# Performance work log

Hardware: AMD Instinct MI355X
Metric: run time of the kernel (lower is better)

## Reference

```python
import jax, jax.numpy as jnp
import numpy as np

N_IM, N_OBJ = 16, 16          # images, objects per image
D_IN = 2048                    # obj_pair_feat_dim
PER_IM = N_OBJ * (N_OBJ + 1) // 2   # obj boxes + union boxes per image
N_BOX = N_IM * PER_IM               # 2176
N_PAIR = N_IM * N_OBJ * (N_OBJ - 1) # is_ex=True -> 2*C(n,2) per image = 3840
NUM_REL = 3


def setup_inputs() -> dict:
    rng = np.random.default_rng(0)
    H, W = 600.0, 800.0
    boxes = np.zeros((N_BOX, 5), np.float32)
    o1i, o2i, ui, imi = [], [], [], []
    for i in range(N_IM):
        off = i * PER_IM
        x1 = rng.uniform(0, W / 2, N_OBJ); y1 = rng.uniform(0, H / 2, N_OBJ)
        bw = rng.uniform(10, W / 2, N_OBJ); bh = rng.uniform(10, H / 2, N_OBJ)
        boxes[off:off + N_OBJ] = np.stack([np.full(N_OBJ, i), x1, y1, x1 + bw, y1 + bh], 1)
        uc = off + N_OBJ
        for a in range(N_OBJ):
            for b in range(a + 1, N_OBJ):
                boxes[uc] = [i, min(x1[a], x1[b]), min(y1[a], y1[b]),
                             max(x1[a] + bw[a], x1[b] + bw[b]), max(y1[a] + bh[a], y1[b] + bh[b])]
                o1i += [off + a, off + b]; o2i += [off + b, off + a]
                ui += [uc, uc]; imi += [i, i]
                uc += 1
    im_info = np.tile(np.array([H, W, 1.0], np.float32), (N_IM, 1))
    key = jax.random.key(0)
    ks = jax.random.split(key, 16)
    lin = lambda k, i, o: jax.random.normal(k, (i, o), jnp.float32) * 0.02
    return dict(
        xs=jax.random.normal(ks[0], (N_PAIR, D_IN), jnp.float32) * 0.1,
        xo=jax.random.normal(ks[1], (N_PAIR, D_IN), jnp.float32) * 0.1,
        xu=jax.random.normal(ks[2], (N_PAIR, D_IN), jnp.float32) * 0.1,
        boxes=jnp.asarray(boxes), im_info=jnp.asarray(im_info),
        o1_idx=jnp.asarray(o1i, jnp.int32), o2_idx=jnp.asarray(o2i, jnp.int32),
        u_idx=jnp.asarray(ui, jnp.int32), img_idx=jnp.asarray(imi, jnp.int32),
        Ws1=lin(ks[3], D_IN, 512), bs1=jnp.zeros(512, jnp.float32),
        Ws2=lin(ks[4], 512, 256), bs2=jnp.zeros(256, jnp.float32),
        Wo1=lin(ks[5], D_IN, 512), bo1=jnp.zeros(512, jnp.float32),
        Wo2=lin(ks[6], 512, 256), bo2=jnp.zeros(256, jnp.float32),
        Wu1=lin(ks[7], D_IN, 512), bu1=jnp.zeros(512, jnp.float32),
        Wu2=lin(ks[8], 512, 256), bu2=jnp.zeros(256, jnp.float32),
        Wc1=lin(ks[9], 256 + 19, 256), bc1=jnp.zeros(256, jnp.float32),
        Wc2=lin(ks[10], 256, NUM_REL), bc2=jnp.zeros(NUM_REL, jnp.float32),
    )


def _mlp(x, W1, b1, W2, b2):
    return jax.nn.relu(jax.nn.relu(x @ W1 + b1) @ W2 + b2)


def _encode_loc(sb, ob, ub, hw):
    # sb/ob/ub: [P,4] (x1,y1,x2,y2); hw: [P,2] (h_i, w_i)
    h_i, w_i = hw[:, 0], hw[:, 1]
    x_s = (sb[:, 0] + sb[:, 2]) / 2.0; y_s = (sb[:, 1] + sb[:, 3]) / 2.0
    w_s = sb[:, 2] - sb[:, 0]; h_s = sb[:, 3] - sb[:, 1]
    x_o = (ob[:, 0] + ob[:, 2]) / 2.0; y_o = (ob[:, 1] + ob[:, 3]) / 2.0
    w_o = ob[:, 2] - ob[:, 0]; h_o = ob[:, 3] - ob[:, 1]
    a_s = w_s * h_s; a_o = w_o * h_o
    a_u = (ub[:, 2] - ub[:, 0]) * (ub[:, 3] - ub[:, 1])
    area = w_i * h_i
    return jnp.stack([
        x_s / w_i, y_s / h_i, (x_s + w_s) / w_i, (y_s + h_s) / h_i, a_s / area,
        x_o / w_i, y_o / h_i, (x_o + w_o) / w_i, (y_o + h_o) / h_i, a_o / area,
        (x_s - x_o) / w_o, (y_s - y_o) / h_o, jnp.log(w_s / w_o), jnp.log(h_s / h_o),
        (x_o - x_s) / w_s, (y_o - y_s) / h_s, jnp.log(w_o / w_s), jnp.log(h_o / h_s),
        a_u / area], axis=1)  # [P,19]


def reference(xs, xo, xu, boxes, im_info, o1_idx, o2_idx, u_idx, img_idx,
              Ws1, bs1, Ws2, bs2, Wo1, bo1, Wo2, bo2, Wu1, bu1, Wu2, bu2,
              Wc1, bc1, Wc2, bc2):
    fs = _mlp(xs, Ws1, bs1, Ws2, bs2)
    fo = _mlp(xo, Wo1, bo1, Wo2, bo2)
    fu = _mlp(xu, Wu1, bu1, Wu2, bu2)
    appear = fu - fo - fs                              # [P,256]
    loc = _encode_loc(boxes[o1_idx, 1:5], boxes[o2_idx, 1:5],
                      boxes[u_idx, 1:5], im_info[img_idx, :2])  # [P,19]
    h = jax.nn.relu(jnp.concatenate([appear, loc], axis=1) @ Wc1 + bc1)
    return h @ Wc2 + bc2                               # [P,num_rel]
```

## Files before the change

### kernel.cpp

```cpp
#include <hip/hip_runtime.h>

#define N_PAIR 3840

typedef short bf16x8 __attribute__((ext_vector_type(8)));
typedef float f32x4 __attribute__((ext_vector_type(4)));

static __device__ __forceinline__ ushort f2bf(float f) {
    uint x = __float_as_uint(f);
    uint r = (x + 0x7FFFu + ((x >> 16) & 1u)) >> 16;
    return (ushort)r;
}
static __device__ __forceinline__ float bf2f(ushort u) {
    return __uint_as_float(((uint)u) << 16);
}

__global__ void transpose_convert(const float* __restrict__ in0,
                                  const float* __restrict__ in1,
                                  const float* __restrict__ in2,
                                  ushort* __restrict__ out,
                                  int K, int N, int Kpad) {
    const float* in = (blockIdx.z == 0) ? in0 : (blockIdx.z == 1 ? in1 : in2);
    ushort* o = out + (size_t)blockIdx.z * N * Kpad;
    __shared__ float tile[64][65];
    int k0 = blockIdx.x * 64, n0 = blockIdx.y * 64;
    int t = threadIdx.x;
    int r = t >> 2, c4 = (t & 3) * 16;
#pragma unroll
    for (int i = 0; i < 16; i++) {
        int k = k0 + r, n = n0 + c4 + i;
        tile[r][c4 + i] = (k < K && n < N) ? in[(size_t)k * N + n] : 0.f;
    }
    __syncthreads();
#pragma unroll
    for (int i = 0; i < 16; i++) {
        int n = n0 + r, k = k0 + c4 + i;
        if (n < N && k < Kpad) o[(size_t)n * Kpad + k] = f2bf(tile[c4 + i][r]);
    }
}

__global__ void transpose_convert2(const float* __restrict__ Ws2,
                                   const float* __restrict__ Wo2,
                                   const float* __restrict__ Wu2,
                                   const float* __restrict__ Wc1,
                                   ushort* __restrict__ W2T,
                                   ushort* __restrict__ WC1T) {
    int z = blockIdx.z;
    const float* in; ushort* o; int K, N, Kpad;
    if (z < 3) {
        in = (z == 0) ? Ws2 : (z == 1 ? Wo2 : Wu2);
        o = W2T + (size_t)z * 256 * 512; K = 512; N = 256; Kpad = 512;
    } else {
        in = Wc1; o = WC1T; K = 275; N = 256; Kpad = 288;
    }
    __shared__ float tile[64][65];
    int k0 = blockIdx.x * 64, n0 = blockIdx.y * 64;
    int t = threadIdx.x;
    int r = t >> 2, c4 = (t & 3) * 16;
#pragma unroll
    for (int i = 0; i < 16; i++) {
        int k = k0 + r, n = n0 + c4 + i;
        tile[r][c4 + i] = (k < K && n < N) ? in[(size_t)k * N + n] : 0.f;
    }
    __syncthreads();
#pragma unroll
    for (int i = 0; i < 16; i++) {
        int n = n0 + r, k = k0 + c4 + i;
        if (n < N && k < Kpad) o[(size_t)n * Kpad + k] = f2bf(tile[c4 + i][r]);
    }
}

__device__ __forceinline__ bf16x8 frag_ld(const ushort* __restrict__ lds, int row, int colbyte) {
    int off = (row << 7) + (colbyte ^ ((row & 7) << 4));
    return *reinterpret_cast<const bf16x8*>(reinterpret_cast<const char*>(lds) + off);
}
__device__ __forceinline__ bf16x8 frag32_ld(const ushort* __restrict__ lds, int row, int colbyte) {
    int off = (row << 6) + (colbyte ^ ((row & 3) << 4));
    return *reinterpret_cast<const bf16x8*>(reinterpret_cast<const char*>(lds) + off);
}

__global__ __launch_bounds__(256) void gemm1(const float* __restrict__ xs,
                                             const float* __restrict__ xo,
                                             const float* __restrict__ xu,
                                             const ushort* __restrict__ w1t,
                                             const float* __restrict__ b_s,
                                             const float* __restrict__ b_o,
                                             const float* __restrict__ b_u,
                                             ushort* __restrict__ h1out) {
    int br = blockIdx.z;
    const float* x = br == 0 ? xs : (br == 1 ? xo : xu);
    const ushort* wt = w1t + (size_t)br * 512 * 2048;
    const float* bias = br == 0 ? b_s : (br == 1 ? b_o : b_u);
    ushort* out = h1out + (size_t)br * 3840 * 512;

    __shared__ ushort As[2][64 * 64];
    __shared__ ushort Bs[2][128 * 64];
    int t = threadIdx.x, lane = t & 63, wid = t >> 6;
    int wr = wid >> 1, wc = wid & 1;
    int m0 = blockIdx.x * 64, n0 = blockIdx.y * 128;
    const float* asrc = x + (size_t)m0 * 2048;
    const ushort* bsrc = wt + (size_t)n0 * 2048;

    int ar = t >> 2, ac = (t & 3) * 16;
    float4 pa[4];
    bf16x8 pb[4];

    auto issue = [&](int kt) {
        const float4* g = reinterpret_cast<const float4*>(asrc + (size_t)ar * 2048 + kt + ac);
#pragma unroll
        for (int i = 0; i < 4; i++) pa[i] = g[i];
#pragma unroll
        for (int it = 0; it < 4; it++) {
            int e = (it * 256 + t) * 8;
            int rr = e >> 6, cc = e & 63;
            pb[it] = *reinterpret_cast<const bf16x8*>(bsrc + (size_t)rr * 2048 + kt + cc);
        }
    };
    auto commit = [&](int buf) {
        union { bf16x8 v; ushort us[8]; } p0, p1;
#pragma unroll
        for (int i = 0; i < 4; i++) {
            p0.us[i] = f2bf(pa[0][i]); p0.us[4 + i] = f2bf(pa[1][i]);
            p1.us[i] = f2bf(pa[2][i]); p1.us[4 + i] = f2bf(pa[3][i]);
        }
        char* ab = reinterpret_cast<char*>(&As[buf][0]);
        int off0 = (ar << 7) + (((ac) << 1) ^ ((ar & 7) << 4));
        int off1 = (ar << 7) + (((ac + 8) << 1) ^ ((ar & 7) << 4));
        *reinterpret_cast<bf16x8*>(ab + off0) = p0.v;
        *reinterpret_cast<bf16x8*>(ab + off1) = p1.v;
        char* bb = reinterpret_cast<char*>(&Bs[buf][0]);
#pragma unroll
        for (int it = 0; it < 4; it++) {
            int e = (it * 256 + t) * 8;
            int rr = e >> 6, cc = e & 63;
            int off = (rr << 7) + ((cc << 1) ^ ((rr & 7) << 4));
            *reinterpret_cast<bf16x8*>(bb + off) = pb[it];
        }
    };

    f32x4 acc[2][4] = {};
    issue(0);
    commit(0);
    __syncthreads();
    int cur = 0;
    for (int kt = 0; kt < 2048; kt += 64) {
        int nxt = kt + 64;
        if (nxt < 2048) issue(nxt);
#pragma unroll
        for (int kk = 0; kk < 64; kk += 32) {
            int cb = (kk + ((lane >> 4) << 3)) << 1;
            bf16x8 a[2], b[4];
#pragma unroll
            for (int i = 0; i < 2; i++) a[i] = frag_ld(&As[cur][0], wr * 32 + i * 16 + (lane & 15), cb);
#pragma unroll
            for (int f = 0; f < 4; f++) b[f] = frag_ld(&Bs[cur][0], wc * 64 + f * 16 + (lane & 15), cb);
#pragma unroll
            for (int i = 0; i < 2; i++)
#pragma unroll
                for (int j = 0; j < 4; j++)
                    acc[i][j] = __builtin_amdgcn_mfma_f32_16x16x32_bf16(a[i], b[j], acc[i][j], 0, 0, 0);
        }
        if (nxt < 2048) commit(cur ^ 1);
        __syncthreads();
        cur ^= 1;
    }
    int rb = m0 + wr * 32 + ((lane >> 4) << 2);
    int cb0 = n0 + wc * 64 + (lane & 15);
#pragma unroll
    for (int j = 0; j < 4; j++) {
        int col = cb0 + j * 16;
        float bv = bias[col];
#pragma unroll
        for (int i = 0; i < 2; i++)
#pragma unroll
            for (int q = 0; q < 4; q++) {
                int row = rb + i * 16 + q;
                float v = acc[i][j][q] + bv;
                v = v > 0.f ? v : 0.f;
                out[(size_t)row * 512 + col] = f2bf(v);
            }
    }
}

__global__ __launch_bounds__(256) void gemm2(const ushort* __restrict__ h1,
                                             const ushort* __restrict__ w2t,
                                             const float* __restrict__ b_s,
                                             const float* __restrict__ b_o,
                                             const float* __restrict__ b_u,
                                             ushort* __restrict__ h2br) {
    int br = blockIdx.z;
    const ushort* A = h1 + (size_t)br * 3840 * 512;
    const ushort* B = w2t + (size_t)br * 256 * 512;
    const float* bias = br == 0 ? b_s : (br == 1 ? b_o : b_u);
    ushort* out = h2br + (size_t)br * 3840 * 256;

    __shared__ ushort As[2][64 * 64];
    __shared__ ushort Bs[2][128 * 64];
    int t = threadIdx.x, lane = t & 63, wid = t >> 6;
    int wr = wid >> 1, wc = wid & 1;
    int m0 = blockIdx.x * 64, n0 = blockIdx.y * 128;
    const ushort* asrc = A + (size_t)m0 * 512;
    const ushort* bsrc = B + (size_t)n0 * 512;

    int ar = t >> 2, ac = (t & 3) * 16;
    bf16x8 pa[2], pb[4];
    auto issue = [&](int kt) {
        const bf16x8* g = reinterpret_cast<const bf16x8*>(asrc + (size_t)ar * 512 + kt + ac);
        pa[0] = g[0]; pa[1] = g[1];
#pragma unroll
        for (int it = 0; it < 4; it++) {
            int e = (it * 256 + t) * 8;
            int rr = e >> 6, cc = e & 63;
            pb[it] = *reinterpret_cast<const bf16x8*>(bsrc + (size_t)rr * 512 + kt + cc);
        }
    };
    auto commit = [&](int buf) {
        char* ab = reinterpret_cast<char*>(&As[buf][0]);
        int off0 = (ar << 7) + ((ac << 1) ^ ((ar & 7) << 4));
        int off1 = (ar << 7) + (((ac + 8) << 1) ^ ((ar & 7) << 4));
        *reinterpret_cast<bf16x8*>(ab + off0) = pa[0];
        *reinterpret_cast<bf16x8*>(ab + off1) = pa[1];
        char* bb = reinterpret_cast<char*>(&Bs[buf][0]);
#pragma unroll
        for (int it = 0; it < 4; it++) {
            int e = (it * 256 + t) * 8;
            int rr = e >> 6, cc = e & 63;
            int off = (rr << 7) + ((cc << 1) ^ ((rr & 7) << 4));
            *reinterpret_cast<bf16x8*>(bb + off) = pb[it];
        }
    };

    f32x4 acc[2][4] = {};
    issue(0);
    commit(0);
    __syncthreads();
    int cur = 0;
    for (int kt = 0; kt < 512; kt += 64) {
        int nxt = kt + 64;
        if (nxt < 512) issue(nxt);
#pragma unroll
        for (int kk = 0; kk < 64; kk += 32) {
            int cb = (kk + ((lane >> 4) << 3)) << 1;
            bf16x8 a[2], b[4];
#pragma unroll
            for (int i = 0; i < 2; i++) a[i] = frag_ld(&As[cur][0], wr * 32 + i * 16 + (lane & 15), cb);
#pragma unroll
            for (int f = 0; f < 4; f++) b[f] = frag_ld(&Bs[cur][0], wc * 64 + f * 16 + (lane & 15), cb);
#pragma unroll
            for (int i = 0; i < 2; i++)
#pragma unroll
                for (int j = 0; j < 4; j++)
                    acc[i][j] = __builtin_amdgcn_mfma_f32_16x16x32_bf16(a[i], b[j], acc[i][j], 0, 0, 0);
        }
        if (nxt < 512) commit(cur ^ 1);
        __syncthreads();
        cur ^= 1;
    }
    int rb = m0 + wr * 32 + ((lane >> 4) << 2);
    int cb0 = n0 + wc * 64 + (lane & 15);
#pragma unroll
    for (int j = 0; j < 4; j++) {
        int col = cb0 + j * 16;
        float bv = bias[col];
#pragma unroll
        for (int i = 0; i < 2; i++)
#pragma unroll
            for (int q = 0; q < 4; q++) {
                int row = rb + i * 16 + q;
                float v = acc[i][j][q] + bv;
                v = v > 0.f ? v : 0.f;
                out[(size_t)row * 256 + col] = f2bf(v);
            }
    }
}

__global__ void appear_pack(const ushort* __restrict__ h2br,
                            ushort* __restrict__ hin,
                            const float* __restrict__ boxes,
                            const float* __restrict__ im_info,
                            const int* __restrict__ o1, const int* __restrict__ o2,
                            const int* __restrict__ u, const int* __restrict__ im) {
    int i = blockIdx.x * 256 + threadIdx.x;
    if (i < N_PAIR * 32) {
        int p = i >> 5, ch = (i & 31) * 8;
        const ushort* ps = h2br + (size_t)p * 256 + ch;
        bf16x8 vs = *reinterpret_cast<const bf16x8*>(ps);
        bf16x8 vo = *reinterpret_cast<const bf16x8*>(ps + (size_t)3840 * 256);
        bf16x8 vu = *reinterpret_cast<const bf16x8*>(ps + (size_t)2 * 3840 * 256);
        union { bf16x8 v; ushort us[8]; } r;
#pragma unroll
        for (int j = 0; j < 8; j++)
            r.us[j] = f2bf(bf2f(((ushort)vu[j])) - bf2f(((ushort)vo[j])) - bf2f(((ushort)vs[j])));
        *reinterpret_cast<bf16x8*>(hin + (size_t)p * 288 + ch) = r.v;
    }
    if (blockIdx.x < 15) {
        int p = blockIdx.x * 256 + threadIdx.x;
        const float* sb = boxes + 5 * o1[p] + 1;
        const float* ob = boxes + 5 * o2[p] + 1;
        const float* ub = boxes + 5 * u[p] + 1;
        const float* ii = im_info + 3 * im[p];
        float hi = ii[0], wi = ii[1];
        float x_s = (sb[0] + sb[2]) * 0.5f, y_s = (sb[1] + sb[3]) * 0.5f;
        float w_s = sb[2] - sb[0], h_s = sb[3] - sb[1];
        float x_o = (ob[0] + ob[2]) * 0.5f, y_o = (ob[1] + ob[3]) * 0.5f;
        float w_o = ob[2] - ob[0], h_o = ob[3] - ob[1];
        float a_s = w_s * h_s, a_o = w_o * h_o;
        float a_u = (ub[2] - ub[0]) * (ub[3] - ub[1]);
        float area = wi * hi;
        float f[19];
        f[0] = x_s / wi;            f[1] = y_s / hi;
        f[2] = (x_s + w_s) / wi;    f[3] = (y_s + h_s) / hi;
        f[4] = a_s / area;
        f[5] = x_o / wi;            f[6] = y_o / hi;
        f[7] = (x_o + w_o) / wi;    f[8] = (y_o + h_o) / hi;
        f[9] = a_o / area;
        f[10] = (x_s - x_o) / w_o;  f[11] = (y_s - y_o) / h_o;
        f[12] = logf(w_s / w_o);    f[13] = logf(h_s / h_o);
        f[14] = (x_o - x_s) / w_s;  f[15] = (y_o - y_s) / h_s;
        f[16] = logf(w_o / w_s);    f[17] = logf(h_o / h_s);
        f[18] = a_u / area;
        ushort* row = hin + (size_t)p * 288 + 256;
#pragma unroll
        for (int k = 0; k < 19; k++) row[k] = f2bf(f[k]);
#pragma unroll
        for (int k = 19; k < 32; k++) row[k] = 0;
    }
}

__global__ __launch_bounds__(256) void gemm3(const ushort* __restrict__ hin,
                                             const ushort* __restrict__ wc1t,
                                             const float* __restrict__ bc1,
                                             ushort* __restrict__ h2) {
    __shared__ ushort As[2][64 * 32];
    __shared__ ushort Bs[2][128 * 32];
    int t = threadIdx.x, lane = t & 63, wid = t >> 6;
    int wr = wid >> 1, wc = wid & 1;
    int m0 = blockIdx.x * 64, n0 = blockIdx.y * 128;
    const ushort* asrc = hin + (size_t)m0 * 288;
    const ushort* bsrc = wc1t + (size_t)n0 * 288;

    int ar = t >> 2, ac = (t & 3) * 8;
    bf16x8 pa, pb[2];
    auto issue = [&](int kt) {
        pa = *reinterpret_cast<const bf16x8*>(asrc + (size_t)ar * 288 + kt + ac);
#pragma unroll
        for (int it = 0; it < 2; it++) {
            int e = (it * 256 + t) * 8;
            int rr = e >> 5, cc = e & 31;
            pb[it] = *reinterpret_cast<const bf16x8*>(bsrc + (size_t)rr * 288 + kt + cc);
        }
    };
    auto commit = [&](int buf) {
        char* ab = reinterpret_cast<char*>(&As[buf][0]);
        int off0 = (ar << 6) + ((ac << 1) ^ ((ar & 3) << 4));
        *reinterpret_cast<bf16x8*>(ab + off0) = pa;
        char* bb = reinterpret_cast<char*>(&Bs[buf][0]);
#pragma unroll
        for (int it = 0; it < 2; it++) {
            int e = (it * 256 + t) * 8;
            int rr = e >> 5, cc = e & 31;
            int off = (rr << 6) + ((cc << 1) ^ ((rr & 3) << 4));
            *reinterpret_cast<bf16x8*>(bb + off) = pb[it];
        }
    };

    f32x4 acc[2][4] = {};
    issue(0);
    commit(0);
    __syncthreads();
    int cur = 0;
    for (int kt = 0; kt < 288; kt += 32) {
        int nxt = kt + 32;
        if (nxt < 288) issue(nxt);
        int cb = ((lane >> 4) << 3) << 1;
        bf16x8 a[2], b[4];
#pragma unroll
        for (int i = 0; i < 2; i++) a[i] = frag32_ld(&As[cur][0], wr * 32 + i * 16 + (lane & 15), cb);
#pragma unroll
        for (int f = 0; f < 4; f++) b[f] = frag32_ld(&Bs[cur][0], wc * 64 + f * 16 + (lane & 15), cb);
#pragma unroll
        for (int i = 0; i < 2; i++)
#pragma unroll
            for (int j = 0; j < 4; j++)
                acc[i][j] = __builtin_amdgcn_mfma_f32_16x16x32_bf16(a[i], b[j], acc[i][j], 0, 0, 0);
        if (nxt < 288) commit(cur ^ 1);
        __syncthreads();
        cur ^= 1;
    }
    int rb = m0 + wr * 32 + ((lane >> 4) << 2);
    int cb0 = n0 + wc * 64 + (lane & 15);
#pragma unroll
    for (int j = 0; j < 4; j++) {
        int col = cb0 + j * 16;
        float bv = bc1[col];
#pragma unroll
        for (int i = 0; i < 2; i++)
#pragma unroll
            for (int q = 0; q < 4; q++) {
                int row = rb + i * 16 + q;
                float v = acc[i][j][q] + bv;
                v = v > 0.f ? v : 0.f;
                h2[(size_t)row * 256 + col] = f2bf(v);
            }
    }
}

__global__ void final_fc(const ushort* __restrict__ h2,
                         const float* __restrict__ wc2,
                         const float* __restrict__ bc2,
                         float* __restrict__ out) {
    __shared__ float w[768];
    int t = threadIdx.x;
    for (int i = t; i < 768; i += 256) w[i] = wc2[i];
    __syncthreads();
    int g = t >> 4, l = t & 15;
    int row = blockIdx.x * 16 + g;
    const ushort* hr = h2 + (size_t)row * 256 + l * 16;
    bf16x8 v0 = *reinterpret_cast<const bf16x8*>(hr);
    bf16x8 v1 = *reinterpret_cast<const bf16x8*>(hr + 8);
    float s0 = 0.f, s1 = 0.f, s2 = 0.f;
#pragma unroll
    for (int k = 0; k < 8; k++) {
        float h = bf2f((ushort)v0[k]);
        int c = (l * 16 + k) * 3;
        s0 += h * w[c]; s1 += h * w[c + 1]; s2 += h * w[c + 2];
    }
#pragma unroll
    for (int k = 0; k < 8; k++) {
        float h = bf2f((ushort)v1[k]);
        int c = (l * 16 + 8 + k) * 3;
        s0 += h * w[c]; s1 += h * w[c + 1]; s2 += h * w[c + 2];
    }
#pragma unroll
    for (int m = 1; m < 16; m <<= 1) {
        s0 += __shfl_xor(s0, m);
        s1 += __shfl_xor(s1, m);
        s2 += __shfl_xor(s2, m);
    }
    if (l == 0) {
        out[row * 3 + 0] = s0 + bc2[0];
        out[row * 3 + 1] = s1 + bc2[1];
        out[row * 3 + 2] = s2 + bc2[2];
    }
}

extern "C" void kernel_launch(void* const* d_in, const int* in_sizes, int n_in,
                              void* d_out, int out_size, void* d_ws, size_t ws_size,
                              hipStream_t stream) {
    (void)in_sizes; (void)n_in; (void)out_size; (void)ws_size;
    const float* xs = (const float*)d_in[0];
    const float* xo = (const float*)d_in[1];
    const float* xu = (const float*)d_in[2];
    const float* boxes = (const float*)d_in[3];
    const float* im_info = (const float*)d_in[4];
    const int* o1 = (const int*)d_in[5];
    const int* o2 = (const int*)d_in[6];
    const int* uu = (const int*)d_in[7];
    const int* im = (const int*)d_in[8];
    const float* Ws1 = (const float*)d_in[9];
    const float* bs1 = (const float*)d_in[10];
    const float* Ws2 = (const float*)d_in[11];
    const float* bs2 = (const float*)d_in[12];
    const float* Wo1 = (const float*)d_in[13];
    const float* bo1 = (const float*)d_in[14];
    const float* Wo2 = (const float*)d_in[15];
    const float* bo2 = (const float*)d_in[16];
    const float* Wu1 = (const float*)d_in[17];
    const float* bu1 = (const float*)d_in[18];
    const float* Wu2 = (const float*)d_in[19];
    const float* bu2 = (const float*)d_in[20];
    const float* Wc1 = (const float*)d_in[21];
    const float* bc1 = (const float*)d_in[22];
    const float* Wc2 = (const float*)d_in[23];
    const float* bc2 = (const float*)d_in[24];
    float* out = (float*)d_out;

    ushort* W1T = (ushort*)d_ws;
    ushort* H2BR = W1T;
    ushort* W2T = W1T + (size_t)3 * 512 * 2048;
    ushort* WC1T = W2T + (size_t)3 * 256 * 512;
    ushort* H1 = WC1T + (size_t)256 * 288;
    ushort* HIN = H1 + (size_t)3 * 3840 * 512;
    ushort* H2 = HIN + (size_t)3840 * 288;

    transpose_convert<<<dim3(32, 8, 3), 256, 0, stream>>>(Ws1, Wo1, Wu1, W1T, 2048, 512, 2048);
    transpose_convert2<<<dim3(8, 4, 4), 256, 0, stream>>>(Ws2, Wo2, Wu2, Wc1, W2T, WC1T);
    gemm1<<<dim3(60, 4, 3), 256, 0, stream>>>(xs, xo, xu, W1T, bs1, bo1, bu1, H1);
    gemm2<<<dim3(60, 2, 3), 256, 0, stream>>>(H1, W2T, bs2, bo2, bu2, H2BR);
    appear_pack<<<480, 256, 0, stream>>>(H2BR, HIN, boxes, im_info, o1, o2, uu, im);
    gemm3<<<dim3(60, 2), 256, 0, stream>>>(HIN, WC1T, bc1, H2);
    final_fc<<<240, 256, 0, stream>>>(H2, Wc2, bc2, out);
}
```

Baseline: 105.0 us.

## Remap GEMM blocks XCD-aware and prefetch two K-tiles ahead in registers

Both MLP GEMMs now use a flat 1D grid with a remap so that consecutive blocks on the same XCD (bid&7) cover contiguous tiles of the same branch, aiming for better L2 reuse of A rows and weight tiles. The main loop is also unrolled by two with two register staging sets, so global loads for tile k+2 are issued while tile k is computed, deepening the prefetch distance. This raises register pressure and could lower occupancy.

```diff
diff --git a/kernel.cpp b/kernel.cpp
--- a/kernel.cpp
+++ b/kernel.cpp
@@ -86,7 +86,11 @@
                                              const float* __restrict__ b_o,
                                              const float* __restrict__ b_u,
                                              ushort* __restrict__ h1out) {
-    int br = blockIdx.z;
+    int bid = blockIdx.x;
+    int w = (bid & 7) * 90 + (bid >> 3);
+    int br = w / 240; int r = w - br * 240;
+    int xt = r >> 2, yt = r & 3;
+
     const float* x = br == 0 ? xs : (br == 1 ? xo : xu);
     const ushort* wt = w1t + (size_t)br * 512 * 2048;
     const float* bias = br == 0 ? b_s : (br == 1 ? b_o : b_u);
@@ -96,72 +100,78 @@
     __shared__ ushort Bs[2][128 * 64];
     int t = threadIdx.x, lane = t & 63, wid = t >> 6;
     int wr = wid >> 1, wc = wid & 1;
-    int m0 = blockIdx.x * 64, n0 = blockIdx.y * 128;
+    int m0 = xt * 64, n0 = yt * 128;
     const float* asrc = x + (size_t)m0 * 2048;
     const ushort* bsrc = wt + (size_t)n0 * 2048;
 
     int ar = t >> 2, ac = (t & 3) * 16;
-    float4 pa[4];
-    bf16x8 pb[4];
-
-    auto issue = [&](int kt) {
-        const float4* g = reinterpret_cast<const float4*>(asrc + (size_t)ar * 2048 + kt + ac);
-#pragma unroll
-        for (int i = 0; i < 4; i++) pa[i] = g[i];
-#pragma unroll
-        for (int it = 0; it < 4; it++) {
-            int e = (it * 256 + t) * 8;
-            int rr = e >> 6, cc = e & 63;
-            pb[it] = *reinterpret_cast<const bf16x8*>(bsrc + (size_t)rr * 2048 + kt + cc);
-        }
-    };
-    auto commit = [&](int buf) {
-        union { bf16x8 v; ushort us[8]; } p0, p1;
-#pragma unroll
-        for (int i = 0; i < 4; i++) {
-            p0.us[i] = f2bf(pa[0][i]); p0.us[4 + i] = f2bf(pa[1][i]);
-            p1.us[i] = f2bf(pa[2][i]); p1.us[4 + i] = f2bf(pa[3][i]);
-        }
-        char* ab = reinterpret_cast<char*>(&As[buf][0]);
-        int off0 = (ar << 7) + (((ac) << 1) ^ ((ar & 7) << 4));
-        int off1 = (ar << 7) + (((ac + 8) << 1) ^ ((ar & 7) << 4));
-        *reinterpret_cast<bf16x8*>(ab + off0) = p0.v;
-        *reinterpret_cast<bf16x8*>(ab + off1) = p1.v;
-        char* bb = reinterpret_cast<char*>(&Bs[buf][0]);
-#pragma unroll
-        for (int it = 0; it < 4; it++) {
-            int e = (it * 256 + t) * 8;
-            int rr = e >> 6, cc = e & 63;
-            int off = (rr << 7) + ((cc << 1) ^ ((rr & 7) << 4));
-            *reinterpret_cast<bf16x8*>(bb + off) = pb[it];
-        }
-    };
+
+    float4 pa0[4], pa1[4];
+    bf16x8 pb0[4], pb1[4];
+
+#define G1_ISSUE(PA, PB, KT)                                                              \
+    {                                                                                     \
+        const float4* g = reinterpret_cast<const float4*>(asrc + (size_t)ar * 2048 + (KT) + ac); \
+        PA[0] = g[0]; PA[1] = g[1]; PA[2] = g[2]; PA[3] = g[3];                           \
+        _Pragma("unroll")                                                                 \
+        for (int it = 0; it < 4; it++) {                                                  \
+            int e = (it * 256 + t) * 8;                                                   \
+            int rr = e >> 6, cc = e & 63;                                                 \
+            PB[it] = *reinterpret_cast<const bf16x8*>(bsrc + (size_t)rr * 2048 + (KT) + cc); \
+        }                                                                                 \
+    }
+#define G1_COMMIT(PA, PB, BUF)                                                            \
+    {                                                                                     \
+        union { bf16x8 v; ushort us[8]; } p0, p1;                                         \
+        _Pragma("unroll")                                                                 \
+        for (int i = 0; i < 4; i++) {                                                     \
+            p0.us[i] = f2bf(PA[0][i]); p0.us[4 + i] = f2bf(PA[1][i]);                     \
+            p1.us[i] = f2bf(PA[2][i]); p1.us[4 + i] = f2bf(PA[3][i]);                     \
+        }                                                                                 \
+        char* ab = reinterpret_cast<char*>(&As[BUF][0]);                                  \
+        int off0 = (ar << 7) + ((ac << 1) ^ ((ar & 7) << 4));                             \
+        int off1 = (ar << 7) + (((ac + 8) << 1) ^ ((ar & 7) << 4));                       \
+        *reinterpret_cast<bf16x8*>(ab + off0) = p0.v;                                     \
+        *reinterpret_cast<bf16x8*>(ab + off1) = p1.v;                                     \
+        char* bb = reinterpret_cast<char*>(&Bs[BUF][0]);                                  \
+        _Pragma("unroll")                                                                 \
+        for (int it = 0; it < 4; it++) {                                                  \
+            int e = (it * 256 + t) * 8;                                                   \
+            int rr = e >> 6, cc = e & 63;                                                 \
+            int off = (rr << 7) + ((cc << 1) ^ ((rr & 7) << 4));                          \
+            *reinterpret_cast<bf16x8*>(bb + off) = PB[it];                                \
+        }                                                                                 \
+    }
+#define G1_MFMA(BUF)                                                                      \
+    _Pragma("unroll")                                                                     \
+    for (int kk = 0; kk < 64; kk += 32) {                                                 \
+        int cb = (kk + ((lane >> 4) << 3)) << 1;                                          \
+        bf16x8 a[2], b[4];                                                                \
+        _Pragma("unroll")                                                                 \
+        for (int i = 0; i < 2; i++) a[i] = frag_ld(&As[BUF][0], wr * 32 + i * 16 + (lane & 15), cb); \
+        _Pragma("unroll")                                                                 \
+        for (int f = 0; f < 4; f++) b[f] = frag_ld(&Bs[BUF][0], wc * 64 + f * 16 + (lane & 15), cb); \
+        _Pragma("unroll")                                                                 \
+        for (int i = 0; i < 2; i++)                                                       \
+            _Pragma("unroll")                                                             \
+            for (int j = 0; j < 4; j++)                                                   \
+                acc[i][j] = __builtin_amdgcn_mfma_f32_16x16x32_bf16(a[i], b[j], acc[i][j], 0, 0, 0); \
+    }
 
     f32x4 acc[2][4] = {};
-    issue(0);
-    commit(0);
+    G1_ISSUE(pa1, pb1, 0)
+    G1_COMMIT(pa1, pb1, 0)
+    G1_ISSUE(pa0, pb0, 64)
     __syncthreads();
-    int cur = 0;
-    for (int kt = 0; kt < 2048; kt += 64) {
-        int nxt = kt + 64;
-        if (nxt < 2048) issue(nxt);
-#pragma unroll
-        for (int kk = 0; kk < 64; kk += 32) {
-            int cb = (kk + ((lane >> 4) << 3)) << 1;
-            bf16x8 a[2], b[4];
-#pragma unroll
-            for (int i = 0; i < 2; i++) a[i] = frag_ld(&As[cur][0], wr * 32 + i * 16 + (lane & 15), cb);
-#pragma unroll
-            for (int f = 0; f < 4; f++) b[f] = frag_ld(&Bs[cur][0], wc * 64 + f * 16 + (lane & 15), cb);
-#pragma unroll
-            for (int i = 0; i < 2; i++)
-#pragma unroll
-                for (int j = 0; j < 4; j++)
-                    acc[i][j] = __builtin_amdgcn_mfma_f32_16x16x32_bf16(a[i], b[j], acc[i][j], 0, 0, 0);
-        }
-        if (nxt < 2048) commit(cur ^ 1);
+    for (int kt = 0; kt < 2048; kt += 128) {
+        if (kt + 128 < 2048) G1_ISSUE(pa1, pb1, kt + 128)
+        G1_MFMA(0)
+        if (kt + 64 < 2048) G1_COMMIT(pa0, pb0, 1)
         __syncthreads();
-        cur ^= 1;
+        if (kt + 192 < 2048) G1_ISSUE(pa0, pb0, kt + 192)
+        G1_MFMA(1)
+        if (kt + 128 < 2048) G1_COMMIT(pa1, pb1, 0)
+        __syncthreads();
     }
     int rb = m0 + wr * 32 + ((lane >> 4) << 2);
     int cb0 = n0 + wc * 64 + (lane & 15);
@@ -179,6 +189,9 @@
                 out[(size_t)row * 512 + col] = f2bf(v);
             }
     }
+#undef G1_ISSUE
+#undef G1_COMMIT
+#undef G1_MFMA
 }
 
 __global__ __launch_bounds__(256) void gemm2(const ushort* __restrict__ h1,
@@ -187,7 +200,11 @@
                                              const float* __restrict__ b_o,
                                              const float* __restrict__ b_u,
                                              ushort* __restrict__ h2br) {
-    int br = blockIdx.z;
+    int bid = blockIdx.x;
+    int w = (bid & 7) * 45 + (bid >> 3);
+    int br = w / 120; int r = w - br * 120;
+    int xt = r >> 1, yt = r & 1;
+
     const ushort* A = h1 + (size_t)br * 3840 * 512;
     const ushort* B = w2t + (size_t)br * 256 * 512;
     const float* bias = br == 0 ? b_s : (br == 1 ? b_o : b_u);
@@ -197,63 +214,70 @@
     __shared__ ushort Bs[2][128 * 64];
     int t = threadIdx.x, lane = t & 63, wid = t >> 6;
     int wr = wid >> 1, wc = wid & 1;
-    int m0 = blockIdx.x * 64, n0 = blockIdx.y * 128;
+    int m0 = xt * 64, n0 = yt * 128;
     const ushort* asrc = A + (size_t)m0 * 512;
     const ushort* bsrc = B + (size_t)n0 * 512;
 
     int ar = t >> 2, ac = (t & 3) * 16;
-    bf16x8 pa[2], pb[4];
-    auto issue = [&](int kt) {
-        const bf16x8* g = reinterpret_cast<const bf16x8*>(asrc + (size_t)ar * 512 + kt + ac);
-        pa[0] = g[0]; pa[1] = g[1];
-#pragma unroll
-        for (int it = 0; it < 4; it++) {
-            int e = (it * 256 + t) * 8;
-            int rr = e >> 6, cc = e & 63;
-            pb[it] = *reinterpret_cast<const bf16x8*>(bsrc + (size_t)rr * 512 + kt + cc);
-        }
-    };
-    auto commit = [&](int buf) {
-        char* ab = reinterpret_cast<char*>(&As[buf][0]);
-        int off0 = (ar << 7) + ((ac << 1) ^ ((ar & 7) << 4));
-        int off1 = (ar << 7) + (((ac + 8) << 1) ^ ((ar & 7) << 4));
-        *reinterpret_cast<bf16x8*>(ab + off0) = pa[0];
-        *reinterpret_cast<bf16x8*>(ab + off1) = pa[1];
-        char* bb = reinterpret_cast<char*>(&Bs[buf][0]);
-#pragma unroll
-        for (int it = 0; it < 4; it++) {
-            int e = (it * 256 + t) * 8;
-            int rr = e >> 6, cc = e & 63;
-            int off = (rr << 7) + ((cc << 1) ^ ((rr & 7) << 4));
-            *reinterpret_cast<bf16x8*>(bb + off) = pb[it];
-        }
-    };
+    bf16x8 qa0[2], qa1[2], qb0[4], qb1[4];
+
+#define G2_ISSUE(PA, PB, KT)                                                              \
+    {                                                                                     \
+        const bf16x8* g = reinterpret_cast<const bf16x8*>(asrc + (size_t)ar * 512 + (KT) + ac); \
+        PA[0] = g[0]; PA[1] = g[1];                                                       \
+        _Pragma("unroll")                                                                 \
+        for (int it = 0; it < 4; it++) {                                                  \
+            int e = (it * 256 + t) * 8;                                                   \
+            int rr = e >> 6, cc = e & 63;                                                 \
+            PB[it] = *reinterpret_cast<const bf16x8*>(bsrc + (size_t)rr * 512 + (KT) + cc); \
+        }                                                                                 \
+    }
+#define G2_COMMIT(PA, PB, BUF)                                                            \
+    {                                                                                     \
+        char* ab = reinterpret_cast<char*>(&As[BUF][0]);                                  \
+        int off0 = (ar << 7) + ((ac << 1) ^ ((ar & 7) << 4));                             \
+        int off1 = (ar << 7) + (((ac + 8) << 1) ^ ((ar & 7) << 4));                       \
+        *reinterpret_cast<bf16x8*>(ab + off0) = PA[0];                                    \
+        *reinterpret_cast<bf16x8*>(ab + off1) = PA[1];                                    \
+        char* bb = reinterpret_cast<char*>(&Bs[BUF][0]);                                  \
+        _Pragma("unroll")                                                                 \
+        for (int it = 0; it < 4; it++) {                                                  \
+            int e = (it * 256 + t) * 8;                                                   \
+            int rr = e >> 6, cc = e & 63;                                                 \
+            int off = (rr << 7) + ((cc << 1) ^ ((rr & 7) << 4));                          \
+            *reinterpret_cast<bf16x8*>(bb + off) = PB[it];                                \
+        }                                                                                 \
+    }
+#define G2_MFMA(BUF)                                                                      \
+    _Pragma("unroll")                                                                     \
+    for (int kk = 0; kk < 64; kk += 32) {                                                 \
+        int cb = (kk + ((lane >> 4) << 3)) << 1;                                          \
+        bf16x8 a[2], b[4];                                                                \
+        _Pragma("unroll")                                                                 \
+        for (int i = 0; i < 2; i++) a[i] = frag_ld(&As[BUF][0], wr * 32 + i * 16 + (lane & 15), cb); \
+        _Pragma("unroll")                                                                 \
+        for (int f = 0; f < 4; f++) b[f] = frag_ld(&Bs[BUF][0], wc * 64 + f * 16 + (lane & 15), cb); \
+        _Pragma("unroll")                                                                 \
+        for (int i = 0; i < 2; i++)                                                       \
+            _Pragma("unroll")                                                             \
+            for (int j = 0; j < 4; j++)                                                   \
+                acc[i][j] = __builtin_amdgcn_mfma_f32_16x16x32_bf16(a[i], b[j], acc[i][j], 0, 0, 0); \
+    }
 
     f32x4 acc[2][4] = {};
-    issue(0);
-    commit(0);
+    G2_ISSUE(qa1, qb1, 0)
+    G2_COMMIT(qa1, qb1, 0)
+    G2_ISSUE(qa0, qb0, 64)
     __syncthreads();
-    int cur = 0;
-    for (int kt = 0; kt < 512; kt += 64) {
-        int nxt = kt + 64;
-        if (nxt < 512) issue(nxt);
-#pragma unroll
-        for (int kk = 0; kk < 64; kk += 32) {
-            int cb = (kk + ((lane >> 4) << 3)) << 1;
-            bf16x8 a[2], b[4];
-#pragma unroll
-            for (int i = 0; i < 2; i++) a[i] = frag_ld(&As[cur][0], wr * 32 + i * 16 + (lane & 15), cb);
-#pragma unroll
-            for (int f = 0; f < 4; f++) b[f] = frag_ld(&Bs[cur][0], wc * 64 + f * 16 + (lane & 15), cb);
-#pragma unroll
-            for (int i = 0; i < 2; i++)
-#pragma unroll
-                for (int j = 0; j < 4; j++)
-                    acc[i][j] = __builtin_amdgcn_mfma_f32_16x16x32_bf16(a[i], b[j], acc[i][j], 0, 0, 0);
-        }
-        if (nxt < 512) commit(cur ^ 1);
+    for (int kt = 0; kt < 512; kt += 128) {
+        if (kt + 128 < 512) G2_ISSUE(qa1, qb1, kt + 128)
+        G2_MFMA(0)
+        if (kt + 64 < 512) G2_COMMIT(qa0, qb0, 1)
         __syncthreads();
-        cur ^= 1;
+        if (kt + 192 < 512) G2_ISSUE(qa0, qb0, kt + 192)
+        G2_MFMA(1)
+        if (kt + 128 < 512) G2_COMMIT(qa1, qb1, 0)
+        __syncthreads();
     }
     int rb = m0 + wr * 32 + ((lane >> 4) << 2);
     int cb0 = n0 + wc * 64 + (lane & 15);
@@ -271,6 +295,9 @@
                 out[(size_t)row * 256 + col] = f2bf(v);
             }
     }
+#undef G2_ISSUE
+#undef G2_COMMIT
+#undef G2_MFMA
 }
 
 __global__ void appear_pack(const ushort* __restrict__ h2br,
@@ -484,8 +511,8 @@
 
     transpose_convert<<<dim3(32, 8, 3), 256, 0, stream>>>(Ws1, Wo1, Wu1, W1T, 2048, 512, 2048);
     transpose_convert2<<<dim3(8, 4, 4), 256, 0, stream>>>(Ws2, Wo2, Wu2, Wc1, W2T, WC1T);
-    gemm1<<<dim3(60, 4, 3), 256, 0, stream>>>(xs, xo, xu, W1T, bs1, bo1, bu1, H1);
-    gemm2<<<dim3(60, 2, 3), 256, 0, stream>>>(H1, W2T, bs2, bo2, bu2, H2BR);
+    gemm1<<<720, 256, 0, stream>>>(xs, xo, xu, W1T, bs1, bo1, bu1, H1);
+    gemm2<<<360, 256, 0, stream>>>(H1, W2T, bs2, bo2, bu2, H2BR);
     appear_pack<<<480, 256, 0, stream>>>(H2BR, HIN, boxes, im_info, o1, o2, uu, im);
     gemm3<<<dim3(60, 2), 256, 0, stream>>>(HIN, WC1T, bc1, H2);
     final_fc<<<240, 256, 0, stream>>>(H2, Wc2, bc2, out);
```

Measured after the change: 97.22 us. -7.4%, faster.
